# Optimization experiments

Hardware: AMD Instinct MI355X
Metric: run time of the kernel (lower is better)

The kernel has to match this reference:

```python
import jax, jax.numpy as jnp
import numpy as np

MAX_DEG = 6


def neighbor_lookup(atoms, edges, maskvalue, include_self):
    # atoms: (B, A, F), edges: (B, A, D) with -1 padding
    B, A, F = atoms.shape
    D = edges.shape[-1]
    mask = edges >= 0
    idx = jnp.where(mask, edges, 0).reshape(B, A * D)
    g = jnp.take_along_axis(atoms, idx[:, :, None], axis=1).reshape(B, A, D, F)
    g = jnp.where(mask[..., None], g, maskvalue)
    if include_self:
        g = jnp.concatenate([atoms[:, :, None, :], g], axis=2)  # (B,A,D+1,F)
    return g


def graph_conv(atoms, bonds, edges, W, b):
    # W: (MAX_DEG, F_in+BF, C), b: (MAX_DEG, C)
    deg = (edges >= 0).sum(-1)  # (B, A)
    summed_atoms = neighbor_lookup(atoms, edges, 0.0, True).sum(2)  # self + neighbors
    summed_bonds = bonds.sum(2)
    feats = jnp.concatenate([summed_atoms, summed_bonds], axis=-1)
    out = jnp.zeros(feats.shape[:2] + (W.shape[-1],), feats.dtype)
    for d in range(MAX_DEG):  # small fixed loop over degrees
        h = jax.nn.relu(feats @ W[d] + b[d])
        out = out + jnp.where((deg == d)[..., None], h, 0.0)
    return out


def graph_pool(atoms, edges):
    g = neighbor_lookup(atoms, edges, -jnp.inf, True)  # self included -> finite max
    return g.max(axis=2)


def graph_output(atoms, bonds, edges, Wo, bo):
    deg = (edges >= 0).sum(-1)
    feats = jnp.concatenate([atoms, bonds.sum(2)], axis=-1)
    out = jax.nn.softmax(feats @ Wo + bo, axis=-1)
    mask = (deg != 0)[..., None]  # zero out padded atoms
    return jnp.where(mask, out, 0.0).sum(axis=1)  # (B, hid)


def setup_inputs():
    key = jax.random.key(0)
    ks = jax.random.split(key, 16)
    B, A, D = 4096, 64, 6
    AF, BF, H = 37, 6, 128
    s = lambda k, sh: (jax.random.normal(k, sh, jnp.float32) * 0.05)
    return {
        "atoms": jax.random.normal(ks[0], (B, A, AF), jnp.float32),
        "bonds": jax.random.normal(ks[1], (B, A, D, BF), jnp.float32),
        "edges": jax.random.randint(ks[2], (B, A, D), -1, A),
        "W1": s(ks[3], (MAX_DEG, AF + BF, H)),
        "b1": s(ks[4], (MAX_DEG, H)),
        "W2": s(ks[5], (MAX_DEG, H + BF, H)),
        "b2": s(ks[6], (MAX_DEG, H)),
        "Wo": s(ks[7], (H + BF, H)),
        "bo": s(ks[8], (H,)),
        "Wm1": s(ks[9], (H, H // 2)),
        "bm1": s(ks[10], (H // 2,)),
        "Wm2": s(ks[11], (H // 2, H // 4)),
        "bm2": s(ks[12], (H // 4,)),
        "Wm3": s(ks[13], (H // 4, 1)),
        "bm3": s(ks[14], (1,)),
    }


def reference(atoms, bonds, edges, W1, b1, W2, b2, Wo, bo, Wm1, bm1, Wm2, bm2, Wm3, bm3):
    x = graph_conv(atoms, bonds, edges, W1, b1)
    x = graph_pool(x, edges)
    x = graph_conv(x, bonds, edges, W2, b2)
    x = graph_pool(x, edges)
    fp = graph_output(x, bonds, edges, Wo, bo)
    h = jax.nn.relu(fp @ Wm1 + bm1)
    h = jax.nn.relu(h @ Wm2 + bm2)
    out = (h @ Wm3 + bm3).squeeze()  # (B,)
    return out
```

## Files before the change

### kernel.cpp

```cpp
#include <hip/hip_runtime.h>
#include <math.h>


__device__ __forceinline__ float4 max4(float4 a, float4 b) {
  return make_float4(fmaxf(a.x, b.x), fmaxf(a.y, b.y), fmaxf(a.z, b.z), fmaxf(a.w, b.w));
}

__device__ __forceinline__ float4 nbr_max(const float4* sx4, const int* se, int a, int c4) {
  float4 m = sx4[a * 32 + c4];
#pragma unroll
  for (int d = 0; d < 6; ++d) {
    int e = se[a * 6 + d];
    if (e >= 0) m = max4(m, sx4[e * 32 + c4]);
  }
  return m;
}

__device__ __forceinline__ float4 nbr_sum(const float4* sx4, const int* se, int a, int c4) {
  float4 s = sx4[a * 32 + c4];
#pragma unroll
  for (int d = 0; d < 6; ++d) {
    int e = se[a * 6 + d];
    if (e >= 0) {
      float4 v = sx4[e * 32 + c4];
      s.x += v.x; s.y += v.y; s.z += v.z; s.w += v.w;
    }
  }
  return s;
}

__device__ __forceinline__ float4 nbr_wmax(const float4* sx4, const int* se, const int* sdeg,
                                           int a, int c4) {
  float4 m = make_float4(0.f, 0.f, 0.f, 0.f);
  if (sdeg[a] < 6) m = max4(m, sx4[a * 32 + c4]);
#pragma unroll
  for (int d = 0; d < 6; ++d) {
    int e = se[a * 6 + d];
    if (e >= 0 && sdeg[e] < 6) m = max4(m, sx4[e * 32 + c4]);
  }
  return m;
}

__global__ __launch_bounds__(256, 4) void qsar_fused(
    const float* __restrict__ atoms, const float* __restrict__ bonds,
    const int* __restrict__ edges,
    const float* __restrict__ W1, const float* __restrict__ b1,
    const float* __restrict__ W2, const float* __restrict__ b2,
    const float* __restrict__ Wo, const float* __restrict__ bo,
    const float* __restrict__ Wm1, const float* __restrict__ bm1,
    const float* __restrict__ Wm2, const float* __restrict__ bm2,
    const float* __restrict__ Wm3, const float* __restrict__ bm3,
    float* __restrict__ out)
{
  const int b    = blockIdx.x;
  const int tid  = threadIdx.x;
  const int wid  = tid >> 6;
  const int hid  = tid >> 5;
  const int hl   = tid & 31;

  __shared__ float s_x[64 * 128];
  __shared__ float s_sa[16 * 38];
  __shared__ float s_bsum[64 * 8];
  __shared__ int   s_edges[64 * 6];
  __shared__ int   s_deg[64];
  __shared__ int   s_work[64];
  __shared__ int   s_perm[64];
  __shared__ float s_rsum[64];
  __shared__ int   s_nwork, s_na, s_nz;

  float4* sx4  = reinterpret_cast<float4*>(s_x);
  float*  s_fp = s_sa;
  float*  s_h1 = s_sa + 256;
  float*  s_h2 = s_sa + 320;

  {
    const int* ge = edges + (size_t)b * (64 * 6);
    for (int i = tid; i < 64 * 6; i += 256) s_edges[i] = ge[i];
    const float* gb = bonds + (size_t)b * (64 * 36);
    for (int i = tid; i < 64 * 6; i += 256) {
      int a = i / 6, f = i - a * 6;
      float s = 0.f;
#pragma unroll
      for (int d = 0; d < 6; ++d) s += gb[a * 36 + d * 6 + f];
      s_bsum[a * 8 + f] = s;
    }
#pragma unroll
    for (int j = 0; j < 8; ++j) sx4[tid + j * 256] = make_float4(0.f, 0.f, 0.f, 0.f);
    if (tid == 0) { s_nwork = 0; s_na = 0; s_nz = 0; }
  }
  __syncthreads();

  if (tid < 64) {
    int dcnt = 0;
#pragma unroll
    for (int d = 0; d < 6; ++d) dcnt += (s_edges[tid * 6 + d] >= 0) ? 1 : 0;
    s_deg[tid] = dcnt;
    if (dcnt < 6) { int p = atomicAdd(&s_nwork, 1); s_work[p] = tid; }
  }
  __syncthreads();

  if (tid < 64) {
    int nzf = (s_deg[tid] < 6) ? 1 : 0;
#pragma unroll
    for (int d = 0; d < 6; ++d) {
      int e = s_edges[tid * 6 + d];
      if (e >= 0 && s_deg[e] < 6) nzf = 1;
    }
    if (nzf) { int p = atomicAdd(&s_na, 1); s_perm[p] = tid; }
    else     { int p = atomicAdd(&s_nz, 1); s_perm[63 - p] = tid; }
  }

  {
    const int nw = s_nwork;
    const float* ga = atoms + (size_t)b * (64 * 37);
    const int c0 = hl * 4;
    for (int cb = 0; cb < nw; cb += 16) {
      const int cnt = (nw - cb < 16) ? (nw - cb) : 16;
      for (int i = tid; i < cnt * 37; i += 256) {
        int wi = i / 37, k = i - wi * 37;
        int a = s_work[cb + wi];
        float f = ga[a * 37 + k];
#pragma unroll
        for (int d = 0; d < 6; ++d) {
          int e = s_edges[a * 6 + d];
          if (e >= 0) f += ga[e * 37 + k];
        }
        s_sa[wi * 38 + k] = f;
      }
      __syncthreads();
      for (int w = hid; w < cnt; w += 8) {
        const int a = s_work[cb + w];
        const int d = s_deg[a];
        const float* wp = W1 + d * (43 * 128);
        float4 acc = *reinterpret_cast<const float4*>(&b1[d * 128 + c0]);
#pragma unroll 4
        for (int k = 0; k < 37; ++k) {
          const float f = s_sa[w * 38 + k];
          const float4 w4 = *reinterpret_cast<const float4*>(&wp[k * 128 + c0]);
          acc.x = fmaf(f, w4.x, acc.x); acc.y = fmaf(f, w4.y, acc.y);
          acc.z = fmaf(f, w4.z, acc.z); acc.w = fmaf(f, w4.w, acc.w);
        }
#pragma unroll
        for (int kk = 0; kk < 6; ++kk) {
          const float f = s_bsum[a * 8 + kk];
          const float4 w4 = *reinterpret_cast<const float4*>(&wp[(37 + kk) * 128 + c0]);
          acc.x = fmaf(f, w4.x, acc.x); acc.y = fmaf(f, w4.y, acc.y);
          acc.z = fmaf(f, w4.z, acc.z); acc.w = fmaf(f, w4.w, acc.w);
        }
        *reinterpret_cast<float4*>(&s_x[a * 128 + c0]) =
            make_float4(fmaxf(acc.x, 0.f), fmaxf(acc.y, 0.f),
                        fmaxf(acc.z, 0.f), fmaxf(acc.w, 0.f));
      }
      __syncthreads();
    }
  }
  __syncthreads();

  {
    float4 v0 = nbr_max(sx4, s_edges, (tid + 0 * 256) >> 5, tid & 31);
    float4 v1 = nbr_max(sx4, s_edges, (tid + 1 * 256) >> 5, tid & 31);
    float4 v2 = nbr_max(sx4, s_edges, (tid + 2 * 256) >> 5, tid & 31);
    float4 v3 = nbr_max(sx4, s_edges, (tid + 3 * 256) >> 5, tid & 31);
    float4 v4 = nbr_max(sx4, s_edges, (tid + 4 * 256) >> 5, tid & 31);
    float4 v5 = nbr_max(sx4, s_edges, (tid + 5 * 256) >> 5, tid & 31);
    float4 v6 = nbr_max(sx4, s_edges, (tid + 6 * 256) >> 5, tid & 31);
    float4 v7 = nbr_max(sx4, s_edges, (tid + 7 * 256) >> 5, tid & 31);
    __syncthreads();
    sx4[tid + 0 * 256] = v0; sx4[tid + 1 * 256] = v1;
    sx4[tid + 2 * 256] = v2; sx4[tid + 3 * 256] = v3;
    sx4[tid + 4 * 256] = v4; sx4[tid + 5 * 256] = v5;
    sx4[tid + 6 * 256] = v6; sx4[tid + 7 * 256] = v7;
  }
  __syncthreads();

  {
    const float4 z = make_float4(0.f, 0.f, 0.f, 0.f);
    float4 v0 = z, v1 = z, v2 = z, v3 = z, v4 = z, v5 = z, v6 = z, v7 = z;
    if (s_deg[(tid + 0 * 256) >> 5] < 6) v0 = nbr_sum(sx4, s_edges, (tid + 0 * 256) >> 5, tid & 31);
    if (s_deg[(tid + 1 * 256) >> 5] < 6) v1 = nbr_sum(sx4, s_edges, (tid + 1 * 256) >> 5, tid & 31);
    if (s_deg[(tid + 2 * 256) >> 5] < 6) v2 = nbr_sum(sx4, s_edges, (tid + 2 * 256) >> 5, tid & 31);
    if (s_deg[(tid + 3 * 256) >> 5] < 6) v3 = nbr_sum(sx4, s_edges, (tid + 3 * 256) >> 5, tid & 31);
    if (s_deg[(tid + 4 * 256) >> 5] < 6) v4 = nbr_sum(sx4, s_edges, (tid + 4 * 256) >> 5, tid & 31);
    if (s_deg[(tid + 5 * 256) >> 5] < 6) v5 = nbr_sum(sx4, s_edges, (tid + 5 * 256) >> 5, tid & 31);
    if (s_deg[(tid + 6 * 256) >> 5] < 6) v6 = nbr_sum(sx4, s_edges, (tid + 6 * 256) >> 5, tid & 31);
    if (s_deg[(tid + 7 * 256) >> 5] < 6) v7 = nbr_sum(sx4, s_edges, (tid + 7 * 256) >> 5, tid & 31);
    __syncthreads();
    if (s_deg[(tid + 0 * 256) >> 5] < 6) sx4[tid + 0 * 256] = v0;
    if (s_deg[(tid + 1 * 256) >> 5] < 6) sx4[tid + 1 * 256] = v1;
    if (s_deg[(tid + 2 * 256) >> 5] < 6) sx4[tid + 2 * 256] = v2;
    if (s_deg[(tid + 3 * 256) >> 5] < 6) sx4[tid + 3 * 256] = v3;
    if (s_deg[(tid + 4 * 256) >> 5] < 6) sx4[tid + 4 * 256] = v4;
    if (s_deg[(tid + 5 * 256) >> 5] < 6) sx4[tid + 5 * 256] = v5;
    if (s_deg[(tid + 6 * 256) >> 5] < 6) sx4[tid + 6 * 256] = v6;
    if (s_deg[(tid + 7 * 256) >> 5] < 6) sx4[tid + 7 * 256] = v7;
  }
  __syncthreads();

  {
    const int nw = s_nwork;
    const int c0 = hl * 4;
    for (int w = hid; w < nw; w += 8) {
      const int a = s_work[w];
      const int d = s_deg[a];
      const float* wp = W2 + d * (134 * 128);
      float4 acc = *reinterpret_cast<const float4*>(&b2[d * 128 + c0]);
#pragma unroll 4
      for (int k = 0; k < 128; ++k) {
        const float f = s_x[a * 128 + k];
        const float4 w4 = *reinterpret_cast<const float4*>(&wp[k * 128 + c0]);
        acc.x = fmaf(f, w4.x, acc.x); acc.y = fmaf(f, w4.y, acc.y);
        acc.z = fmaf(f, w4.z, acc.z); acc.w = fmaf(f, w4.w, acc.w);
      }
#pragma unroll
      for (int kk = 0; kk < 6; ++kk) {
        const float f = s_bsum[a * 8 + kk];
        const float4 w4 = *reinterpret_cast<const float4*>(&wp[(128 + kk) * 128 + c0]);
        acc.x = fmaf(f, w4.x, acc.x); acc.y = fmaf(f, w4.y, acc.y);
        acc.z = fmaf(f, w4.z, acc.z); acc.w = fmaf(f, w4.w, acc.w);
      }
      *reinterpret_cast<float4*>(&s_x[a * 128 + c0]) =
          make_float4(fmaxf(acc.x, 0.f), fmaxf(acc.y, 0.f),
                      fmaxf(acc.z, 0.f), fmaxf(acc.w, 0.f));
    }
  }
  __syncthreads();

  {
    float4 v0 = nbr_wmax(sx4, s_edges, s_deg, (tid + 0 * 256) >> 5, tid & 31);
    float4 v1 = nbr_wmax(sx4, s_edges, s_deg, (tid + 1 * 256) >> 5, tid & 31);
    float4 v2 = nbr_wmax(sx4, s_edges, s_deg, (tid + 2 * 256) >> 5, tid & 31);
    float4 v3 = nbr_wmax(sx4, s_edges, s_deg, (tid + 3 * 256) >> 5, tid & 31);
    float4 v4 = nbr_wmax(sx4, s_edges, s_deg, (tid + 4 * 256) >> 5, tid & 31);
    float4 v5 = nbr_wmax(sx4, s_edges, s_deg, (tid + 5 * 256) >> 5, tid & 31);
    float4 v6 = nbr_wmax(sx4, s_edges, s_deg, (tid + 6 * 256) >> 5, tid & 31);
    float4 v7 = nbr_wmax(sx4, s_edges, s_deg, (tid + 7 * 256) >> 5, tid & 31);
    __syncthreads();
    sx4[tid + 0 * 256] = v0; sx4[tid + 1 * 256] = v1;
    sx4[tid + 2 * 256] = v2; sx4[tid + 3 * 256] = v3;
    sx4[tid + 4 * 256] = v4; sx4[tid + 5 * 256] = v5;
    sx4[tid + 6 * 256] = v6; sx4[tid + 7 * 256] = v7;
  }
  __syncthreads();

  {
    const int cg = tid & 31, ag = hid;
    const int c0 = cg * 4;
    const int na = s_na;
    const int nr = (na + 31) >> 5;
    for (int j = 0; j < nr; ++j) {
      const int sl = j * 32 + ag * 4;
      const int at0 = s_perm[sl + 0], at1 = s_perm[sl + 1];
      const int at2 = s_perm[sl + 2], at3 = s_perm[sl + 3];
      float a00 = 0.f, a01 = 0.f, a02 = 0.f, a03 = 0.f;
      float a10 = 0.f, a11 = 0.f, a12 = 0.f, a13 = 0.f;
      float a20 = 0.f, a21 = 0.f, a22 = 0.f, a23 = 0.f;
      float a30 = 0.f, a31 = 0.f, a32 = 0.f, a33 = 0.f;
      if (j * 32 + wid * 8 < na) {
#pragma unroll 4
        for (int k = 0; k < 128; ++k) {
          const float4 w4 = *reinterpret_cast<const float4*>(Wo + k * 128 + c0);
          const float f0 = s_x[at0 * 128 + k], f1 = s_x[at1 * 128 + k];
          const float f2 = s_x[at2 * 128 + k], f3 = s_x[at3 * 128 + k];
          a00 = fmaf(f0, w4.x, a00); a01 = fmaf(f0, w4.y, a01);
          a02 = fmaf(f0, w4.z, a02); a03 = fmaf(f0, w4.w, a03);
          a10 = fmaf(f1, w4.x, a10); a11 = fmaf(f1, w4.y, a11);
          a12 = fmaf(f1, w4.z, a12); a13 = fmaf(f1, w4.w, a13);
          a20 = fmaf(f2, w4.x, a20); a21 = fmaf(f2, w4.y, a21);
          a22 = fmaf(f2, w4.z, a22); a23 = fmaf(f2, w4.w, a23);
          a30 = fmaf(f3, w4.x, a30); a31 = fmaf(f3, w4.y, a31);
          a32 = fmaf(f3, w4.z, a32); a33 = fmaf(f3, w4.w, a33);
        }
#pragma unroll
        for (int kk = 0; kk < 6; ++kk) {
          const float4 w4 = *reinterpret_cast<const float4*>(Wo + (128 + kk) * 128 + c0);
          const float f0 = s_bsum[at0 * 8 + kk], f1 = s_bsum[at1 * 8 + kk];
          const float f2 = s_bsum[at2 * 8 + kk], f3 = s_bsum[at3 * 8 + kk];
          a00 = fmaf(f0, w4.x, a00); a01 = fmaf(f0, w4.y, a01);
          a02 = fmaf(f0, w4.z, a02); a03 = fmaf(f0, w4.w, a03);
          a10 = fmaf(f1, w4.x, a10); a11 = fmaf(f1, w4.y, a11);
          a12 = fmaf(f1, w4.z, a12); a13 = fmaf(f1, w4.w, a13);
          a20 = fmaf(f2, w4.x, a20); a21 = fmaf(f2, w4.y, a21);
          a22 = fmaf(f2, w4.z, a22); a23 = fmaf(f2, w4.w, a23);
          a30 = fmaf(f3, w4.x, a30); a31 = fmaf(f3, w4.y, a31);
          a32 = fmaf(f3, w4.z, a32); a33 = fmaf(f3, w4.w, a33);
        }
      }
      __syncthreads();
      const float4 bo4 = *reinterpret_cast<const float4*>(bo + c0);
      if (sl + 0 < na)
        *reinterpret_cast<float4*>(&s_x[at0 * 128 + c0]) =
            make_float4(a00 + bo4.x, a01 + bo4.y, a02 + bo4.z, a03 + bo4.w);
      if (sl + 1 < na)
        *reinterpret_cast<float4*>(&s_x[at1 * 128 + c0]) =
            make_float4(a10 + bo4.x, a11 + bo4.y, a12 + bo4.z, a13 + bo4.w);
      if (sl + 2 < na)
        *reinterpret_cast<float4*>(&s_x[at2 * 128 + c0]) =
            make_float4(a20 + bo4.x, a21 + bo4.y, a22 + bo4.z, a23 + bo4.w);
      if (sl + 3 < na)
        *reinterpret_cast<float4*>(&s_x[at3 * 128 + c0]) =
            make_float4(a30 + bo4.x, a31 + bo4.y, a32 + bo4.z, a33 + bo4.w);
    }
    const int nz = 64 - na;
    for (int e = tid; e < nz * 128; e += 256) {
      int zi = e >> 7, c = e & 127;
      int a = s_perm[na + zi];
      float acc = bo[c];
#pragma unroll
      for (int kk = 0; kk < 6; ++kk)
        acc = fmaf(s_bsum[a * 8 + kk], Wo[(128 + kk) * 128 + c], acc);
      s_x[a * 128 + c] = acc;
    }
  }
  __syncthreads();

  {
    const int a = tid >> 2, q = tid & 3;
    float* base = &s_x[a * 128 + q * 32];
    const float4 v0 = *reinterpret_cast<const float4*>(base + ((0 + tid) & 7) * 4);
    const float4 v1 = *reinterpret_cast<const float4*>(base + ((1 + tid) & 7) * 4);
    const float4 v2 = *reinterpret_cast<const float4*>(base + ((2 + tid) & 7) * 4);
    const float4 v3 = *reinterpret_cast<const float4*>(base + ((3 + tid) & 7) * 4);
    const float4 v4 = *reinterpret_cast<const float4*>(base + ((4 + tid) & 7) * 4);
    const float4 v5 = *reinterpret_cast<const float4*>(base + ((5 + tid) & 7) * 4);
    const float4 v6 = *reinterpret_cast<const float4*>(base + ((6 + tid) & 7) * 4);
    const float4 v7 = *reinterpret_cast<const float4*>(base + ((7 + tid) & 7) * 4);
    float mx = fmaxf(fmaxf(fmaxf(v0.x, v0.y), fmaxf(v0.z, v0.w)),
                     fmaxf(fmaxf(v1.x, v1.y), fmaxf(v1.z, v1.w)));
    mx = fmaxf(mx, fmaxf(fmaxf(fmaxf(v2.x, v2.y), fmaxf(v2.z, v2.w)),
                         fmaxf(fmaxf(v3.x, v3.y), fmaxf(v3.z, v3.w))));
    mx = fmaxf(mx, fmaxf(fmaxf(fmaxf(v4.x, v4.y), fmaxf(v4.z, v4.w)),
                         fmaxf(fmaxf(v5.x, v5.y), fmaxf(v5.z, v5.w))));
    mx = fmaxf(mx, fmaxf(fmaxf(fmaxf(v6.x, v6.y), fmaxf(v6.z, v6.w)),
                         fmaxf(fmaxf(v7.x, v7.y), fmaxf(v7.z, v7.w))));
    mx = fmaxf(mx, __shfl_xor(mx, 1));
    mx = fmaxf(mx, __shfl_xor(mx, 2));
    float sm = 0.f;
    float4 e0, e1, e2, e3, e4, e5, e6, e7;
    e0.x = __expf(v0.x - mx); e0.y = __expf(v0.y - mx); e0.z = __expf(v0.z - mx); e0.w = __expf(v0.w - mx);
    e1.x = __expf(v1.x - mx); e1.y = __expf(v1.y - mx); e1.z = __expf(v1.z - mx); e1.w = __expf(v1.w - mx);
    e2.x = __expf(v2.x - mx); e2.y = __expf(v2.y - mx); e2.z = __expf(v2.z - mx); e2.w = __expf(v2.w - mx);
    e3.x = __expf(v3.x - mx); e3.y = __expf(v3.y - mx); e3.z = __expf(v3.z - mx); e3.w = __expf(v3.w - mx);
    e4.x = __expf(v4.x - mx); e4.y = __expf(v4.y - mx); e4.z = __expf(v4.z - mx); e4.w = __expf(v4.w - mx);
    e5.x = __expf(v5.x - mx); e5.y = __expf(v5.y - mx); e5.z = __expf(v5.z - mx); e5.w = __expf(v5.w - mx);
    e6.x = __expf(v6.x - mx); e6.y = __expf(v6.y - mx); e6.z = __expf(v6.z - mx); e6.w = __expf(v6.w - mx);
    e7.x = __expf(v7.x - mx); e7.y = __expf(v7.y - mx); e7.z = __expf(v7.z - mx); e7.w = __expf(v7.w - mx);
    sm += e0.x + e0.y + e0.z + e0.w; sm += e1.x + e1.y + e1.z + e1.w;
    sm += e2.x + e2.y + e2.z + e2.w; sm += e3.x + e3.y + e3.z + e3.w;
    sm += e4.x + e4.y + e4.z + e4.w; sm += e5.x + e5.y + e5.z + e5.w;
    sm += e6.x + e6.y + e6.z + e6.w; sm += e7.x + e7.y + e7.z + e7.w;
    *reinterpret_cast<float4*>(base + ((0 + tid) & 7) * 4) = e0;
    *reinterpret_cast<float4*>(base + ((1 + tid) & 7) * 4) = e1;
    *reinterpret_cast<float4*>(base + ((2 + tid) & 7) * 4) = e2;
    *reinterpret_cast<float4*>(base + ((3 + tid) & 7) * 4) = e3;
    *reinterpret_cast<float4*>(base + ((4 + tid) & 7) * 4) = e4;
    *reinterpret_cast<float4*>(base + ((5 + tid) & 7) * 4) = e5;
    *reinterpret_cast<float4*>(base + ((6 + tid) & 7) * 4) = e6;
    *reinterpret_cast<float4*>(base + ((7 + tid) & 7) * 4) = e7;
    sm += __shfl_xor(sm, 1);
    sm += __shfl_xor(sm, 2);
    if (q == 0) s_rsum[a] = (s_deg[a] != 0) ? (1.f / sm) : 0.f;
  }
  __syncthreads();

  {
    const int c = tid & 127, half = tid >> 7;
    float s = 0.f;
    for (int a2 = half * 32; a2 < half * 32 + 32; ++a2)
      s = fmaf(s_x[a2 * 128 + c], s_rsum[a2], s);
    s_fp[half * 128 + c] = s;
  }
  __syncthreads();
  if (tid < 128) s_fp[tid] += s_fp[128 + tid];
  __syncthreads();

  if (tid < 64) {
    float acc = bm1[tid];
    for (int k = 0; k < 128; ++k) acc = fmaf(s_fp[k], Wm1[k * 64 + tid], acc);
    s_h1[tid] = fmaxf(acc, 0.f);
  }
  __syncthreads();
  if (tid < 32) {
    float acc = bm2[tid];
    for (int k = 0; k < 64; ++k) acc = fmaf(s_h1[k], Wm2[k * 32 + tid], acc);
    s_h2[tid] = fmaxf(acc, 0.f);
  }
  __syncthreads();
  if (tid < 64) {
    float p = (tid < 32) ? s_h2[tid] * Wm3[tid] : 0.f;
#pragma unroll
    for (int off = 32; off > 0; off >>= 1) p += __shfl_xor(p, off);
    if (tid == 0) out[b] = p + bm3[0];
  }
}

extern "C" void kernel_launch(void* const* d_in, const int* in_sizes, int n_in,
                              void* d_out, int out_size, void* d_ws, size_t ws_size,
                              hipStream_t stream) {
  const float* atoms = (const float*)d_in[0];
  const float* bonds = (const float*)d_in[1];
  const int*   edges = (const int*)d_in[2];
  const float* W1  = (const float*)d_in[3];
  const float* b1  = (const float*)d_in[4];
  const float* W2  = (const float*)d_in[5];
  const float* b2  = (const float*)d_in[6];
  const float* Wo  = (const float*)d_in[7];
  const float* bo  = (const float*)d_in[8];
  const float* Wm1 = (const float*)d_in[9];
  const float* bm1 = (const float*)d_in[10];
  const float* Wm2 = (const float*)d_in[11];
  const float* bm2 = (const float*)d_in[12];
  const float* Wm3 = (const float*)d_in[13];
  const float* bm3 = (const float*)d_in[14];
  float* out = (float*)d_out;

  const int B = out_size;
  qsar_fused<<<dim3(B), dim3(256), 0, stream>>>(
      atoms, bonds, edges, W1, b1, W2, b2, Wo, bo,
      Wm1, bm1, Wm2, bm2, Wm3, bm3, out);
}
```

Baseline: 245.8 us.

## Group work atoms by degree and tile eight atoms per wave in conv/output matmuls

Atoms with degree below 6 are bucketed by degree, so each wavefront handles one degree and computes eight atoms at once with float2 weight columns per lane. This cuts global weight loads per atom and removes the 16-atom chunking and its extra barriers in the first conv. The output projection uses the same eight-atom register tile and drops the separate bias-only path for the remaining atoms. The risk is load imbalance: most work atoms tend to share one degree, which can leave one wave doing most of the conv work while the other waves idle, and register pressure rises.

```diff
diff --git a/kernel.cpp b/kernel.cpp
--- a/kernel.cpp
+++ b/kernel.cpp
@@ -1,6 +1,16 @@
 #include <hip/hip_runtime.h>
 #include <math.h>
 
+
+#define ACC16_FMA(W2V) \
+  a0x = fmaf(f0, (W2V).x, a0x); a0y = fmaf(f0, (W2V).y, a0y); \
+  a1x = fmaf(f1, (W2V).x, a1x); a1y = fmaf(f1, (W2V).y, a1y); \
+  a2x = fmaf(f2, (W2V).x, a2x); a2y = fmaf(f2, (W2V).y, a2y); \
+  a3x = fmaf(f3, (W2V).x, a3x); a3y = fmaf(f3, (W2V).y, a3y); \
+  a4x = fmaf(f4, (W2V).x, a4x); a4y = fmaf(f4, (W2V).y, a4y); \
+  a5x = fmaf(f5, (W2V).x, a5x); a5y = fmaf(f5, (W2V).y, a5y); \
+  a6x = fmaf(f6, (W2V).x, a6x); a6y = fmaf(f6, (W2V).y, a6y); \
+  a7x = fmaf(f7, (W2V).x, a7x); a7y = fmaf(f7, (W2V).y, a7y);
 
 __device__ __forceinline__ float4 max4(float4 a, float4 b) {
   return make_float4(fmaxf(a.x, b.x), fmaxf(a.y, b.y), fmaxf(a.z, b.z), fmaxf(a.w, b.w));
@@ -52,20 +62,20 @@
     const float* __restrict__ Wm3, const float* __restrict__ bm3,
     float* __restrict__ out)
 {
-  const int b    = blockIdx.x;
-  const int tid  = threadIdx.x;
-  const int wid  = tid >> 6;
-  const int hid  = tid >> 5;
-  const int hl   = tid & 31;
+  const int b   = blockIdx.x;
+  const int tid = threadIdx.x;
+  const int wv  = tid >> 6;
+  const int ln  = tid & 63;
 
   __shared__ float s_x[64 * 128];
-  __shared__ float s_sa[16 * 38];
+  __shared__ float s_sa[64 * 38];
   __shared__ float s_bsum[64 * 8];
   __shared__ int   s_edges[64 * 6];
   __shared__ int   s_deg[64];
   __shared__ int   s_work[64];
   __shared__ int   s_perm[64];
   __shared__ float s_rsum[64];
+  __shared__ int   s_dcnt[6], s_dfill[6], s_doff[7];
   __shared__ int   s_nwork, s_na, s_nz;
 
   float4* sx4  = reinterpret_cast<float4*>(s_x);
@@ -86,7 +96,8 @@
     }
 #pragma unroll
     for (int j = 0; j < 8; ++j) sx4[tid + j * 256] = make_float4(0.f, 0.f, 0.f, 0.f);
-    if (tid == 0) { s_nwork = 0; s_na = 0; s_nz = 0; }
+    if (tid < 6) s_dcnt[tid] = 0;
+    if (tid == 0) { s_na = 0; s_nz = 0; }
   }
   __syncthreads();
 
@@ -95,10 +106,17 @@
 #pragma unroll
     for (int d = 0; d < 6; ++d) dcnt += (s_edges[tid * 6 + d] >= 0) ? 1 : 0;
     s_deg[tid] = dcnt;
-    if (dcnt < 6) { int p = atomicAdd(&s_nwork, 1); s_work[p] = tid; }
-  }
-  __syncthreads();
-
+    if (dcnt < 6) atomicAdd(&s_dcnt[dcnt], 1);
+  }
+  __syncthreads();
+
+  if (tid == 0) {
+    int off = 0;
+#pragma unroll
+    for (int d = 0; d < 6; ++d) { s_doff[d] = off; s_dfill[d] = off; off += s_dcnt[d]; }
+    s_doff[6] = off;
+    s_nwork = off;
+  }
   if (tid < 64) {
     int nzf = (s_deg[tid] < 6) ? 1 : 0;
 #pragma unroll
@@ -109,49 +127,88 @@
     if (nzf) { int p = atomicAdd(&s_na, 1); s_perm[p] = tid; }
     else     { int p = atomicAdd(&s_nz, 1); s_perm[63 - p] = tid; }
   }
+  __syncthreads();
+
+  if (tid < 64 && s_deg[tid] < 6) {
+    int p = atomicAdd(&s_dfill[s_deg[tid]], 1);
+    s_work[p] = tid;
+  }
+  __syncthreads();
 
   {
     const int nw = s_nwork;
     const float* ga = atoms + (size_t)b * (64 * 37);
-    const int c0 = hl * 4;
-    for (int cb = 0; cb < nw; cb += 16) {
-      const int cnt = (nw - cb < 16) ? (nw - cb) : 16;
-      for (int i = tid; i < cnt * 37; i += 256) {
-        int wi = i / 37, k = i - wi * 37;
-        int a = s_work[cb + wi];
-        float f = ga[a * 37 + k];
-#pragma unroll
-        for (int d = 0; d < 6; ++d) {
-          int e = s_edges[a * 6 + d];
-          if (e >= 0) f += ga[e * 37 + k];
+    for (int i = tid; i < nw * 37; i += 256) {
+      int wi = i / 37, k = i - wi * 37;
+      int a = s_work[wi];
+      float f = ga[a * 37 + k];
+#pragma unroll
+      for (int d = 0; d < 6; ++d) {
+        int e = s_edges[a * 6 + d];
+        if (e >= 0) f += ga[e * 37 + k];
+      }
+      s_sa[wi * 38 + k] = f;
+    }
+  }
+  __syncthreads();
+
+  {
+    for (int pass = 0; pass < 2; ++pass) {
+      const int d = wv + pass * 4;
+      if (d <= 5) {
+        const int beg = s_doff[d], e = s_doff[d + 1];
+        if (beg < e) {
+          const float2* wp2 = reinterpret_cast<const float2*>(W1 + (size_t)d * (43 * 128));
+          const float2 bb = reinterpret_cast<const float2*>(b1 + (size_t)d * 128)[ln];
+          for (int j = beg; j < e; j += 8) {
+            const int c1 = (j + 1 < e) ? j + 1 : j, c2 = (j + 2 < e) ? j + 2 : j;
+            const int c3 = (j + 3 < e) ? j + 3 : j, c4 = (j + 4 < e) ? j + 4 : j;
+            const int c5 = (j + 5 < e) ? j + 5 : j, c6 = (j + 6 < e) ? j + 6 : j;
+            const int c7 = (j + 7 < e) ? j + 7 : j;
+            const int at0 = s_work[j],  at1 = s_work[c1], at2 = s_work[c2], at3 = s_work[c3];
+            const int at4 = s_work[c4], at5 = s_work[c5], at6 = s_work[c6], at7 = s_work[c7];
+            float a0x = bb.x, a0y = bb.y, a1x = bb.x, a1y = bb.y;
+            float a2x = bb.x, a2y = bb.y, a3x = bb.x, a3y = bb.y;
+            float a4x = bb.x, a4y = bb.y, a5x = bb.x, a5y = bb.y;
+            float a6x = bb.x, a6y = bb.y, a7x = bb.x, a7y = bb.y;
+            float f0, f1, f2, f3, f4, f5, f6, f7;
+#pragma unroll 2
+            for (int k = 0; k < 37; ++k) {
+              const float2 w = wp2[k * 64 + ln];
+              f0 = s_sa[j  * 38 + k]; f1 = s_sa[c1 * 38 + k];
+              f2 = s_sa[c2 * 38 + k]; f3 = s_sa[c3 * 38 + k];
+              f4 = s_sa[c4 * 38 + k]; f5 = s_sa[c5 * 38 + k];
+              f6 = s_sa[c6 * 38 + k]; f7 = s_sa[c7 * 38 + k];
+              ACC16_FMA(w)
+            }
+#pragma unroll
+            for (int kk = 0; kk < 6; ++kk) {
+              const float2 w = wp2[(37 + kk) * 64 + ln];
+              f0 = s_bsum[at0 * 8 + kk]; f1 = s_bsum[at1 * 8 + kk];
+              f2 = s_bsum[at2 * 8 + kk]; f3 = s_bsum[at3 * 8 + kk];
+              f4 = s_bsum[at4 * 8 + kk]; f5 = s_bsum[at5 * 8 + kk];
+              f6 = s_bsum[at6 * 8 + kk]; f7 = s_bsum[at7 * 8 + kk];
+              ACC16_FMA(w)
+            }
+            *reinterpret_cast<float2*>(&s_x[at0 * 128 + 2 * ln]) =
+                make_float2(fmaxf(a0x, 0.f), fmaxf(a0y, 0.f));
+            if (j + 1 < e) *reinterpret_cast<float2*>(&s_x[at1 * 128 + 2 * ln]) =
+                make_float2(fmaxf(a1x, 0.f), fmaxf(a1y, 0.f));
+            if (j + 2 < e) *reinterpret_cast<float2*>(&s_x[at2 * 128 + 2 * ln]) =
+                make_float2(fmaxf(a2x, 0.f), fmaxf(a2y, 0.f));
+            if (j + 3 < e) *reinterpret_cast<float2*>(&s_x[at3 * 128 + 2 * ln]) =
+                make_float2(fmaxf(a3x, 0.f), fmaxf(a3y, 0.f));
+            if (j + 4 < e) *reinterpret_cast<float2*>(&s_x[at4 * 128 + 2 * ln]) =
+                make_float2(fmaxf(a4x, 0.f), fmaxf(a4y, 0.f));
+            if (j + 5 < e) *reinterpret_cast<float2*>(&s_x[at5 * 128 + 2 * ln]) =
+                make_float2(fmaxf(a5x, 0.f), fmaxf(a5y, 0.f));
+            if (j + 6 < e) *reinterpret_cast<float2*>(&s_x[at6 * 128 + 2 * ln]) =
+                make_float2(fmaxf(a6x, 0.f), fmaxf(a6y, 0.f));
+            if (j + 7 < e) *reinterpret_cast<float2*>(&s_x[at7 * 128 + 2 * ln]) =
+                make_float2(fmaxf(a7x, 0.f), fmaxf(a7y, 0.f));
+          }
         }
-        s_sa[wi * 38 + k] = f;
       }
-      __syncthreads();
-      for (int w = hid; w < cnt; w += 8) {
-        const int a = s_work[cb + w];
-        const int d = s_deg[a];
-        const float* wp = W1 + d * (43 * 128);
-        float4 acc = *reinterpret_cast<const float4*>(&b1[d * 128 + c0]);
-#pragma unroll 4
-        for (int k = 0; k < 37; ++k) {
-          const float f = s_sa[w * 38 + k];
-          const float4 w4 = *reinterpret_cast<const float4*>(&wp[k * 128 + c0]);
-          acc.x = fmaf(f, w4.x, acc.x); acc.y = fmaf(f, w4.y, acc.y);
-          acc.z = fmaf(f, w4.z, acc.z); acc.w = fmaf(f, w4.w, acc.w);
-        }
-#pragma unroll
-        for (int kk = 0; kk < 6; ++kk) {
-          const float f = s_bsum[a * 8 + kk];
-          const float4 w4 = *reinterpret_cast<const float4*>(&wp[(37 + kk) * 128 + c0]);
-          acc.x = fmaf(f, w4.x, acc.x); acc.y = fmaf(f, w4.y, acc.y);
-          acc.z = fmaf(f, w4.z, acc.z); acc.w = fmaf(f, w4.w, acc.w);
-        }
-        *reinterpret_cast<float4*>(&s_x[a * 128 + c0]) =
-            make_float4(fmaxf(acc.x, 0.f), fmaxf(acc.y, 0.f),
-                        fmaxf(acc.z, 0.f), fmaxf(acc.w, 0.f));
-      }
-      __syncthreads();
     }
   }
   __syncthreads();
@@ -197,30 +254,62 @@
   __syncthreads();
 
   {
-    const int nw = s_nwork;
-    const int c0 = hl * 4;
-    for (int w = hid; w < nw; w += 8) {
-      const int a = s_work[w];
-      const int d = s_deg[a];
-      const float* wp = W2 + d * (134 * 128);
-      float4 acc = *reinterpret_cast<const float4*>(&b2[d * 128 + c0]);
-#pragma unroll 4
-      for (int k = 0; k < 128; ++k) {
-        const float f = s_x[a * 128 + k];
-        const float4 w4 = *reinterpret_cast<const float4*>(&wp[k * 128 + c0]);
-        acc.x = fmaf(f, w4.x, acc.x); acc.y = fmaf(f, w4.y, acc.y);
-        acc.z = fmaf(f, w4.z, acc.z); acc.w = fmaf(f, w4.w, acc.w);
+    for (int pass = 0; pass < 2; ++pass) {
+      const int d = wv + pass * 4;
+      if (d <= 5) {
+        const int beg = s_doff[d], e = s_doff[d + 1];
+        if (beg < e) {
+          const float2* wp2 = reinterpret_cast<const float2*>(W2 + (size_t)d * (134 * 128));
+          const float2 bb = reinterpret_cast<const float2*>(b2 + (size_t)d * 128)[ln];
+          for (int j = beg; j < e; j += 8) {
+            const int c1 = (j + 1 < e) ? j + 1 : j, c2 = (j + 2 < e) ? j + 2 : j;
+            const int c3 = (j + 3 < e) ? j + 3 : j, c4 = (j + 4 < e) ? j + 4 : j;
+            const int c5 = (j + 5 < e) ? j + 5 : j, c6 = (j + 6 < e) ? j + 6 : j;
+            const int c7 = (j + 7 < e) ? j + 7 : j;
+            const int at0 = s_work[j],  at1 = s_work[c1], at2 = s_work[c2], at3 = s_work[c3];
+            const int at4 = s_work[c4], at5 = s_work[c5], at6 = s_work[c6], at7 = s_work[c7];
+            float a0x = bb.x, a0y = bb.y, a1x = bb.x, a1y = bb.y;
+            float a2x = bb.x, a2y = bb.y, a3x = bb.x, a3y = bb.y;
+            float a4x = bb.x, a4y = bb.y, a5x = bb.x, a5y = bb.y;
+            float a6x = bb.x, a6y = bb.y, a7x = bb.x, a7y = bb.y;
+            float f0, f1, f2, f3, f4, f5, f6, f7;
+#pragma unroll 2
+            for (int k = 0; k < 128; ++k) {
+              const float2 w = wp2[k * 64 + ln];
+              f0 = s_x[at0 * 128 + k]; f1 = s_x[at1 * 128 + k];
+              f2 = s_x[at2 * 128 + k]; f3 = s_x[at3 * 128 + k];
+              f4 = s_x[at4 * 128 + k]; f5 = s_x[at5 * 128 + k];
+              f6 = s_x[at6 * 128 + k]; f7 = s_x[at7 * 128 + k];
+              ACC16_FMA(w)
+            }
+#pragma unroll
+            for (int kk = 0; kk < 6; ++kk) {
+              const float2 w = wp2[(128 + kk) * 64 + ln];
+              f0 = s_bsum[at0 * 8 + kk]; f1 = s_bsum[at1 * 8 + kk];
+              f2 = s_bsum[at2 * 8 + kk]; f3 = s_bsum[at3 * 8 + kk];
+              f4 = s_bsum[at4 * 8 + kk]; f5 = s_bsum[at5 * 8 + kk];
+              f6 = s_bsum[at6 * 8 + kk]; f7 = s_bsum[at7 * 8 + kk];
+              ACC16_FMA(w)
+            }
+            *reinterpret_cast<float2*>(&s_x[at0 * 128 + 2 * ln]) =
+                make_float2(fmaxf(a0x, 0.f), fmaxf(a0y, 0.f));
+            if (j + 1 < e) *reinterpret_cast<float2*>(&s_x[at1 * 128 + 2 * ln]) =
+                make_float2(fmaxf(a1x, 0.f), fmaxf(a1y, 0.f));
+            if (j + 2 < e) *reinterpret_cast<float2*>(&s_x[at2 * 128 + 2 * ln]) =
+                make_float2(fmaxf(a2x, 0.f), fmaxf(a2y, 0.f));
+            if (j + 3 < e) *reinterpret_cast<float2*>(&s_x[at3 * 128 + 2 * ln]) =
+                make_float2(fmaxf(a3x, 0.f), fmaxf(a3y, 0.f));
+            if (j + 4 < e) *reinterpret_cast<float2*>(&s_x[at4 * 128 + 2 * ln]) =
+                make_float2(fmaxf(a4x, 0.f), fmaxf(a4y, 0.f));
+            if (j + 5 < e) *reinterpret_cast<float2*>(&s_x[at5 * 128 + 2 * ln]) =
+                make_float2(fmaxf(a5x, 0.f), fmaxf(a5y, 0.f));
+            if (j + 6 < e) *reinterpret_cast<float2*>(&s_x[at6 * 128 + 2 * ln]) =
+                make_float2(fmaxf(a6x, 0.f), fmaxf(a6y, 0.f));
+            if (j + 7 < e) *reinterpret_cast<float2*>(&s_x[at7 * 128 + 2 * ln]) =
+                make_float2(fmaxf(a7x, 0.f), fmaxf(a7y, 0.f));
+          }
+        }
       }
-#pragma unroll
-      for (int kk = 0; kk < 6; ++kk) {
-        const float f = s_bsum[a * 8 + kk];
-        const float4 w4 = *reinterpret_cast<const float4*>(&wp[(128 + kk) * 128 + c0]);
-        acc.x = fmaf(f, w4.x, acc.x); acc.y = fmaf(f, w4.y, acc.y);
-        acc.z = fmaf(f, w4.z, acc.z); acc.w = fmaf(f, w4.w, acc.w);
-      }
-      *reinterpret_cast<float4*>(&s_x[a * 128 + c0]) =
-          make_float4(fmaxf(acc.x, 0.f), fmaxf(acc.y, 0.f),
-                      fmaxf(acc.z, 0.f), fmaxf(acc.w, 0.f));
     }
   }
   __syncthreads();
@@ -243,72 +332,48 @@
   __syncthreads();
 
   {
-    const int cg = tid & 31, ag = hid;
-    const int c0 = cg * 4;
     const int na = s_na;
-    const int nr = (na + 31) >> 5;
-    for (int j = 0; j < nr; ++j) {
-      const int sl = j * 32 + ag * 4;
+    const float2* Wof2 = reinterpret_cast<const float2*>(Wo);
+    const float2 bo2 = reinterpret_cast<const float2*>(bo)[ln];
+    for (int r = 0; r < 2; ++r) {
+      const int sl = r * 32 + wv * 8;
       const int at0 = s_perm[sl + 0], at1 = s_perm[sl + 1];
       const int at2 = s_perm[sl + 2], at3 = s_perm[sl + 3];
-      float a00 = 0.f, a01 = 0.f, a02 = 0.f, a03 = 0.f;
-      float a10 = 0.f, a11 = 0.f, a12 = 0.f, a13 = 0.f;
-      float a20 = 0.f, a21 = 0.f, a22 = 0.f, a23 = 0.f;
-      float a30 = 0.f, a31 = 0.f, a32 = 0.f, a33 = 0.f;
-      if (j * 32 + wid * 8 < na) {
-#pragma unroll 4
+      const int at4 = s_perm[sl + 4], at5 = s_perm[sl + 5];
+      const int at6 = s_perm[sl + 6], at7 = s_perm[sl + 7];
+      float a0x = 0.f, a0y = 0.f, a1x = 0.f, a1y = 0.f;
+      float a2x = 0.f, a2y = 0.f, a3x = 0.f, a3y = 0.f;
+      float a4x = 0.f, a4y = 0.f, a5x = 0.f, a5y = 0.f;
+      float a6x = 0.f, a6y = 0.f, a7x = 0.f, a7y = 0.f;
+      float f0, f1, f2, f3, f4, f5, f6, f7;
+      if (sl < na) {
+#pragma unroll 2
         for (int k = 0; k < 128; ++k) {
-          const float4 w4 = *reinterpret_cast<const float4*>(Wo + k * 128 + c0);
-          const float f0 = s_x[at0 * 128 + k], f1 = s_x[at1 * 128 + k];
-          const float f2 = s_x[at2 * 128 + k], f3 = s_x[at3 * 128 + k];
-          a00 = fmaf(f0, w4.x, a00); a01 = fmaf(f0, w4.y, a01);
-          a02 = fmaf(f0, w4.z, a02); a03 = fmaf(f0, w4.w, a03);
-          a10 = fmaf(f1, w4.x, a10); a11 = fmaf(f1, w4.y, a11);
-          a12 = fmaf(f1, w4.z, a12); a13 = fmaf(f1, w4.w, a13);
-          a20 = fmaf(f2, w4.x, a20); a21 = fmaf(f2, w4.y, a21);
-          a22 = fmaf(f2, w4.z, a22); a23 = fmaf(f2, w4.w, a23);
-          a30 = fmaf(f3, w4.x, a30); a31 = fmaf(f3, w4.y, a31);
-          a32 = fmaf(f3, w4.z, a32); a33 = fmaf(f3, w4.w, a33);
-        }
-#pragma unroll
-        for (int kk = 0; kk < 6; ++kk) {
-          const float4 w4 = *reinterpret_cast<const float4*>(Wo + (128 + kk) * 128 + c0);
-          const float f0 = s_bsum[at0 * 8 + kk], f1 = s_bsum[at1 * 8 + kk];
-          const float f2 = s_bsum[at2 * 8 + kk], f3 = s_bsum[at3 * 8 + kk];
-          a00 = fmaf(f0, w4.x, a00); a01 = fmaf(f0, w4.y, a01);
-          a02 = fmaf(f0, w4.z, a02); a03 = fmaf(f0, w4.w, a03);
-          a10 = fmaf(f1, w4.x, a10); a11 = fmaf(f1, w4.y, a11);
-          a12 = fmaf(f1, w4.z, a12); a13 = fmaf(f1, w4.w, a13);
-          a20 = fmaf(f2, w4.x, a20); a21 = fmaf(f2, w4.y, a21);
-          a22 = fmaf(f2, w4.z, a22); a23 = fmaf(f2, w4.w, a23);
-          a30 = fmaf(f3, w4.x, a30); a31 = fmaf(f3, w4.y, a31);
-          a32 = fmaf(f3, w4.z, a32); a33 = fmaf(f3, w4.w, a33);
+          const float2 w = Wof2[k * 64 + ln];
+          f0 = s_x[at0 * 128 + k]; f1 = s_x[at1 * 128 + k];
+          f2 = s_x[at2 * 128 + k]; f3 = s_x[at3 * 128 + k];
+          f4 = s_x[at4 * 128 + k]; f5 = s_x[at5 * 128 + k];
+          f6 = s_x[at6 * 128 + k]; f7 = s_x[at7 * 128 + k];
+          ACC16_FMA(w)
         }
       }
-      __syncthreads();
-      const float4 bo4 = *reinterpret_cast<const float4*>(bo + c0);
-      if (sl + 0 < na)
-        *reinterpret_cast<float4*>(&s_x[at0 * 128 + c0]) =
-            make_float4(a00 + bo4.x, a01 + bo4.y, a02 + bo4.z, a03 + bo4.w);
-      if (sl + 1 < na)
-        *reinterpret_cast<float4*>(&s_x[at1 * 128 + c0]) =
-            make_float4(a10 + bo4.x, a11 + bo4.y, a12 + bo4.z, a13 + bo4.w);
-      if (sl + 2 < na)
-        *reinterpret_cast<float4*>(&s_x[at2 * 128 + c0]) =
-            make_float4(a20 + bo4.x, a21 + bo4.y, a22 + bo4.z, a23 + bo4.w);
-      if (sl + 3 < na)
-        *reinterpret_cast<float4*>(&s_x[at3 * 128 + c0]) =
-            make_float4(a30 + bo4.x, a31 + bo4.y, a32 + bo4.z, a33 + bo4.w);
-    }
-    const int nz = 64 - na;
-    for (int e = tid; e < nz * 128; e += 256) {
-      int zi = e >> 7, c = e & 127;
-      int a = s_perm[na + zi];
-      float acc = bo[c];
-#pragma unroll
-      for (int kk = 0; kk < 6; ++kk)
-        acc = fmaf(s_bsum[a * 8 + kk], Wo[(128 + kk) * 128 + c], acc);
-      s_x[a * 128 + c] = acc;
+#pragma unroll
+      for (int kk = 0; kk < 6; ++kk) {
+        const float2 w = Wof2[(128 + kk) * 64 + ln];
+        f0 = s_bsum[at0 * 8 + kk]; f1 = s_bsum[at1 * 8 + kk];
+        f2 = s_bsum[at2 * 8 + kk]; f3 = s_bsum[at3 * 8 + kk];
+        f4 = s_bsum[at4 * 8 + kk]; f5 = s_bsum[at5 * 8 + kk];
+        f6 = s_bsum[at6 * 8 + kk]; f7 = s_bsum[at7 * 8 + kk];
+        ACC16_FMA(w)
+      }
+      *reinterpret_cast<float2*>(&s_x[at0 * 128 + 2 * ln]) = make_float2(a0x + bo2.x, a0y + bo2.y);
+      *reinterpret_cast<float2*>(&s_x[at1 * 128 + 2 * ln]) = make_float2(a1x + bo2.x, a1y + bo2.y);
+      *reinterpret_cast<float2*>(&s_x[at2 * 128 + 2 * ln]) = make_float2(a2x + bo2.x, a2y + bo2.y);
+      *reinterpret_cast<float2*>(&s_x[at3 * 128 + 2 * ln]) = make_float2(a3x + bo2.x, a3y + bo2.y);
+      *reinterpret_cast<float2*>(&s_x[at4 * 128 + 2 * ln]) = make_float2(a4x + bo2.x, a4y + bo2.y);
+      *reinterpret_cast<float2*>(&s_x[at5 * 128 + 2 * ln]) = make_float2(a5x + bo2.x, a5y + bo2.y);
+      *reinterpret_cast<float2*>(&s_x[at6 * 128 + 2 * ln]) = make_float2(a6x + bo2.x, a6y + bo2.y);
+      *reinterpret_cast<float2*>(&s_x[at7 * 128 + 2 * ln]) = make_float2(a7x + bo2.x, a7y + bo2.y);
     }
   }
   __syncthreads();
```

New measurement: 361.8 us. +47.2%, slower.
